# Kernel tuning notes

Hardware: AMD Instinct MI355X
Metric: run time of the kernel (lower is better)

Reference implementation:

```python
import jax, jax.numpy as jnp
import numpy as np

N_NODES = 100000
N_GRAPHS = 1000
NPG = 100           # nodes per graph (fixed)
N_EDGES = 3200000   # avg degree 32
F_IN = 128
K = 30              # SortAggregation k
N_CLASSES = 10


def setup_inputs() -> dict:
    key = jax.random.key(0)
    ks = jax.random.split(key, 24)
    x = jax.random.normal(ks[0], (N_NODES, F_IN), jnp.float32)
    # edges constrained within each 100-node graph
    g = jax.random.randint(ks[1], (N_EDGES,), 0, N_GRAPHS)
    src = g * NPG + jax.random.randint(ks[2], (N_EDGES,), 0, NPG)
    dst = g * NPG + jax.random.randint(ks[3], (N_EDGES,), 0, NPG)
    edge_index = jnp.stack([src, dst]).astype(jnp.int32)
    batch = jnp.repeat(jnp.arange(N_GRAPHS, dtype=jnp.int32), NPG)

    def lin(k, fi, fo):
        return jax.random.normal(k, (fi, fo), jnp.float32) / np.sqrt(fi)

    return {
        "x": x, "edge_index": edge_index, "batch": batch,
        "W1": lin(ks[4], F_IN, 32), "b1": jnp.zeros((32,), jnp.float32),
        "W2": lin(ks[5], 32, 32),   "b2": jnp.zeros((32,), jnp.float32),
        "W3": lin(ks[6], 32, 32),   "b3": jnp.zeros((32,), jnp.float32),
        "W4": lin(ks[7], 32, 1),    "b4": jnp.zeros((1,), jnp.float32),
        "conv5_w": jax.random.normal(ks[8], (16, 1, 97), jnp.float32) / np.sqrt(97.0),
        "conv5_b": jnp.zeros((16,), jnp.float32),
        "conv6_w": jax.random.normal(ks[9], (32, 16, 5), jnp.float32) / np.sqrt(16 * 5.0),
        "conv6_b": jnp.zeros((32,), jnp.float32),
        "fc1_w": lin(ks[10], 352, 128), "fc1_b": jnp.zeros((128,), jnp.float32),
        "fc2_w": lin(ks[11], 128, N_CLASSES), "fc2_b": jnp.zeros((N_CLASSES,), jnp.float32),
    }


def reference(x, edge_index, batch,
              W1, b1, W2, b2, W3, b3, W4, b4,
              conv5_w, conv5_b, conv6_w, conv6_b,
              fc1_w, fc1_b, fc2_w, fc2_b):
    N = x.shape[0]
    src, dst = edge_index[0], edge_index[1]
    # remove_self_loops -> zero edge weight; GCNConv then re-adds self loops (weight 1)
    w = jnp.where(src == dst, 0.0, 1.0).astype(x.dtype)
    deg = jax.ops.segment_sum(w, dst, num_segments=N) + 1.0  # includes self loop
    dis = jax.lax.rsqrt(deg)
    norm = w * dis[src] * dis[dst]        # per-edge D^-1/2 A D^-1/2
    self_norm = dis * dis                 # self-loop coefficient 1/deg

    def gcn(h, W, b):
        h = h @ W                                   # [N, out]
        agg = jax.ops.segment_sum(norm[:, None] * h[src], dst, num_segments=N)
        return agg + self_norm[:, None] * h + b

    x1 = jnp.tanh(gcn(x, W1, b1))
    x2 = jnp.tanh(gcn(x1, W2, b2))
    x3 = jnp.tanh(gcn(x2, W3, b3))
    x4 = jnp.tanh(gcn(x3, W4, b4))
    h = jnp.concatenate([x1, x2, x3, x4], axis=-1)  # [N, 97]
    C = h.shape[-1]

    # SortAggregation(k=30): per graph, sort nodes by last channel descending, keep top k
    xs = h.reshape(N_GRAPHS, NPG, C)
    order = jnp.argsort(-xs[..., -1], axis=1)[:, :K]            # [B, K]
    pooled = jnp.take_along_axis(xs, order[:, :, None], axis=1)  # [B, K, C]
    y = pooled.reshape(N_GRAPHS, 1, K * C)                       # [B, 1, 2910]

    dn = ('NCH', 'OIH', 'NCH')
    y = jax.lax.conv_general_dilated(y, conv5_w, (97,), 'VALID', dimension_numbers=dn)
    y = jax.nn.relu(y + conv5_b[None, :, None])                  # [B, 16, 30]
    B, Co, L = y.shape
    y = y.reshape(B, Co, L // 2, 2).max(axis=-1)                 # maxpool(2,2) -> [B,16,15]
    y = jax.lax.conv_general_dilated(y, conv6_w, (1,), 'VALID', dimension_numbers=dn)
    y = jax.nn.relu(y + conv6_b[None, :, None])                  # [B, 32, 11]
    y = y.reshape(B, -1)                                         # [B, 352]
    out = jax.nn.relu(y @ fc1_w + fc1_b)                         # dropout = identity (eval)
    return jax.nn.log_softmax(out @ fc2_w + fc2_b, axis=-1)
```

## Files before the change

### kernel.cpp

```cpp
#include <hip/hip_runtime.h>

#define N_GRAPHS_C 1000
#define NPG_C      100
#define N_EDGES_C  3200000
#define KTOP_C     30
#define CAP        4096
#define NB_BUCKET  391

typedef _Float16 f16x8 __attribute__((ext_vector_type(8)));
typedef float    f32x4 __attribute__((ext_vector_type(4)));

__device__ __forceinline__ unsigned packh2(float x, float y) {
    _Float16 hx = (_Float16)x, hy = (_Float16)y;
    return (unsigned)__builtin_bit_cast(unsigned short, hx) |
           ((unsigned)__builtin_bit_cast(unsigned short, hy) << 16);
}

__device__ __forceinline__ float f16b(unsigned v) {
    return (float)__builtin_bit_cast(_Float16, (unsigned short)v);
}

__device__ __forceinline__ float ftanh(float x) {
    float e = __expf(2.0f * x);
    return 1.0f - 2.0f * __builtin_amdgcn_rcpf(e + 1.0f);
}

__device__ __forceinline__ void split8(const float* v, f16x8& h, f16x8& l) {
    #pragma unroll
    for (int j = 0; j < 8; ++j) {
        _Float16 hh = (_Float16)v[j];
        h[j] = hh;
        l[j] = (_Float16)(v[j] - (float)hh);
    }
}


__global__ __launch_bounds__(1024)
void bucket_kernel(const int* __restrict__ src, const int* __restrict__ dst,
                   int* __restrict__ gcur, unsigned short* __restrict__ slots,
                   const float* __restrict__ W1, const float* __restrict__ W2,
                   const float* __restrict__ W3, unsigned* __restrict__ wp) {
    const int tid = threadIdx.x;
    if (blockIdx.x == NB_BUCKET) {
        for (int w = tid; w < 2048; w += 1024) {
            int n = w >> 6, kp = w & 63, k = kp * 2;
            float a = W1[k*32 + n], b = W1[(k+1)*32 + n];
            _Float16 ah = (_Float16)a, bh = (_Float16)b;
            wp[w]        = (unsigned)__builtin_bit_cast(unsigned short, ah) |
                           ((unsigned)__builtin_bit_cast(unsigned short, bh) << 16);
            wp[2048 + w] = packh2(a - (float)ah, b - (float)bh);
        }
        for (int w = tid; w < 512; w += 1024) {
            int n = w >> 4, kp = w & 15, k = kp * 2;
            float a = W2[k*32 + n], b = W2[(k+1)*32 + n];
            _Float16 ah = (_Float16)a, bh = (_Float16)b;
            wp[4096 + w] = (unsigned)__builtin_bit_cast(unsigned short, ah) |
                           ((unsigned)__builtin_bit_cast(unsigned short, bh) << 16);
            wp[4608 + w] = packh2(a - (float)ah, b - (float)bh);
            float a3 = W3[k*32 + n], b3v = W3[(k+1)*32 + n];
            _Float16 a3h = (_Float16)a3, b3h = (_Float16)b3v;
            wp[5120 + w] = (unsigned)__builtin_bit_cast(unsigned short, a3h) |
                           ((unsigned)__builtin_bit_cast(unsigned short, b3h) << 16);
            wp[5632 + w] = packh2(a3 - (float)a3h, b3v - (float)b3h);
        }
        return;
    }

    __shared__ int hist[N_GRAPHS_C];
    const int base = blockIdx.x * 8192;
    for (int i = tid; i < N_GRAPHS_C; i += 1024) hist[i] = 0;
    __syncthreads();

    int g[8]; unsigned short pk[8]; bool v[8];
    #pragma unroll
    for (int k = 0; k < 8; ++k) {
        int e = base + tid + k * 1024;
        v[k] = false;
        if (e < N_EDGES_C) {
            int s = src[e], d = dst[e];
            if (s != d) {
                int gg = s / NPG_C;
                g[k] = gg;
                pk[k] = (unsigned short)(((d - gg * NPG_C) << 7) | (s - gg * NPG_C));
                v[k] = true;
                atomicAdd(&hist[gg], 1);
            }
        }
    }
    __syncthreads();
    for (int i = tid; i < N_GRAPHS_C; i += 1024) {
        int c = hist[i];
        hist[i] = atomicAdd(&gcur[i], c);
    }
    __syncthreads();
    #pragma unroll
    for (int k = 0; k < 8; ++k) {
        if (v[k]) {
            int pos = atomicAdd(&hist[g[k]], 1);
            if (pos < CAP) slots[g[k] * CAP + pos] = pk[k];
        }
    }
}

#define SMEM_WORDS 8496

extern "C" __global__ __launch_bounds__(512, 8)
void dgcnn_kernel(const float* __restrict__ x,
                  const int* __restrict__ gcur, const unsigned short* __restrict__ slots,
                  const unsigned* __restrict__ wp,
                  const float* __restrict__ b1, const float* __restrict__ b2,
                  const float* __restrict__ b3,
                  const float* __restrict__ W4, const float* __restrict__ b4,
                  const float* __restrict__ w5, const float* __restrict__ b5,
                  const float* __restrict__ w6, const float* __restrict__ b6,
                  const float* __restrict__ fw1, const float* __restrict__ fb1,
                  const float* __restrict__ fw2, const float* __restrict__ fb2,
                  float* __restrict__ out)
{
    extern __shared__ unsigned smu[];
    unsigned* planes = smu;
    float* xrows  = (float*)(smu + 4352);
    float* pooled = (float*)(smu + 4352);
    float* dis = (float*)(smu + 7952);
    float* t4  = (float*)(smu + 8064);
    unsigned* t4h = smu + 8168;
    unsigned* t4l = smu + 8232;
    float* sX4 = (float*)(smu + 8296);
    int*   srank = (int*)(smu + 8396);
    float* s5  = (float*)smu;
    float* sPb = s5 + 480;
    float* s6  = s5 + 720;
    float* sO1 = s5 + 1072;
    float* sFc = s5 + 1200;
    float* sZ  = s5 + 1712;

    const int tid = threadIdx.x;
    const int g   = blockIdx.x;
    const int l64 = tid & 63;
    const int wv  = tid >> 6;

    const float* xg = x + (size_t)g * NPG_C * 128;
    const unsigned* w1h = wp;
    const unsigned* w1l = wp + 2048;

    for (int idx = tid; idx < 2600; idx += 512) planes[idx] = 0u;
    if (tid < 12) dis[100 + tid] = 0.f;
    if (tid < 100) srank[tid] = 0;
    __syncthreads();

    {
        int ec = gcur[g]; if (ec > CAP) ec = CAP;
        for (int k = tid; k < ec; k += 512) {
            unsigned e = slots[g * CAP + k];
            unsigned idx = (e >> 7) * 104 + (e & 127);
            atomicAdd(&planes[idx >> 2], 1u << ((idx & 3) * 8));
        }
    }
    __syncthreads();

    if (tid < 400) {
        int row = tid >> 2, part = tid & 3;
        int wb = part * 7, we = (part == 3) ? 26 : wb + 7;
        const unsigned* rw = planes + row * 26;
        unsigned s = 0;
        for (int k = wb; k < we; ++k) {
            unsigned v = rw[k];
            s += (v & 0xffu) + ((v >> 8) & 0xffu) + ((v >> 16) & 0xffu) + (v >> 24);
        }
        atomicAdd(&srank[row], (int)s);
    }
    f16x8 afr[4];
    {
        const int arow = (wv << 4) + (l64 & 15);
        if (wv < 7 && arow < 100) {
            const unsigned* cb = planes + arow * 26 + ((l64 >> 4) << 1);
            #pragma unroll
            for (int ks = 0; ks < 4; ++ks) {
                uint2 cw = *(const uint2*)(cb + ks * 8);
                #pragma unroll
                for (int j = 0; j < 4; ++j) {
                    afr[ks][j]     = (_Float16)(float)((cw.x >> (8*j)) & 255u);
                    afr[ks][4 + j] = (_Float16)(float)((cw.y >> (8*j)) & 255u);
                }
            }
        } else {
            #pragma unroll
            for (int ks = 0; ks < 4; ++ks)
                #pragma unroll
                for (int j = 0; j < 8; ++j) afr[ks][j] = (_Float16)0.f;
        }
    }
    __syncthreads();

    if (tid < 100) dis[tid] = rsqrtf((float)srank[tid] + 1.0f);
    __syncthreads();

    auto packStore = [&](f32x4 c, int n, int r0, float4 dv) {
        float v0 = c[0]*dv.x, v1 = c[1]*dv.y, v2 = c[2]*dv.z, v3 = c[3]*dv.w;
        _Float16 h0=(_Float16)v0, h1=(_Float16)v1, h2=(_Float16)v2, h3=(_Float16)v3;
        uint2 wh, wl;
        wh.x = (unsigned)__builtin_bit_cast(unsigned short,h0) |
               ((unsigned)__builtin_bit_cast(unsigned short,h1) << 16);
        wh.y = (unsigned)__builtin_bit_cast(unsigned short,h2) |
               ((unsigned)__builtin_bit_cast(unsigned short,h3) << 16);
        wl.x = packh2(v0-(float)h0, v1-(float)h1);
        wl.y = packh2(v2-(float)h2, v3-(float)h3);
        *(uint2*)&planes[n*68 + (r0>>1)] = wh;
        *(uint2*)&planes[2176 + n*68 + (r0>>1)] = wl;
    };

    for (int idx = tid; idx < 768; idx += 512) {
        int rw = idx / 12, wd = idx - rw * 12;
        planes[rw * 68 + 56 + wd] = 0u;
    }
    if (wv < 7) {
        f32x4 c0 = {0.f,0.f,0.f,0.f}, c1 = {0.f,0.f,0.f,0.f};
        const int arow = (wv << 4) + (l64 & 15);
        const int kq   = (l64 >> 4) << 3;
        const int bn   = l64 & 15;
        const bool aok = arow < 100;
        #pragma unroll
        for (int kc = 0; kc < 4; ++kc) {
            const int kb = (kc << 5) + kq;
            f16x8 ah, al;
            if (aok) {
                float av[8];
                float4 xa = *(const float4*)&xg[arow*128 + kb];
                float4 xb = *(const float4*)&xg[arow*128 + kb + 4];
                av[0]=xa.x; av[1]=xa.y; av[2]=xa.z; av[3]=xa.w;
                av[4]=xb.x; av[5]=xb.y; av[6]=xb.z; av[7]=xb.w;
                split8(av, ah, al);
            } else {
                #pragma unroll
                for (int j = 0; j < 8; ++j) { ah[j] = (_Float16)0.f; al[j] = (_Float16)0.f; }
            }
            f16x8 b0h = __builtin_bit_cast(f16x8, *(const uint4*)(w1h + bn*64 + (kb>>1)));
            f16x8 b0l = __builtin_bit_cast(f16x8, *(const uint4*)(w1l + bn*64 + (kb>>1)));
            f16x8 b1h = __builtin_bit_cast(f16x8, *(const uint4*)(w1h + (bn+16)*64 + (kb>>1)));
            f16x8 b1l = __builtin_bit_cast(f16x8, *(const uint4*)(w1l + (bn+16)*64 + (kb>>1)));
            c0 = __builtin_amdgcn_mfma_f32_16x16x32_f16(ah, b0h, c0, 0, 0, 0);
            c0 = __builtin_amdgcn_mfma_f32_16x16x32_f16(al, b0h, c0, 0, 0, 0);
            c0 = __builtin_amdgcn_mfma_f32_16x16x32_f16(ah, b0l, c0, 0, 0, 0);
            c1 = __builtin_amdgcn_mfma_f32_16x16x32_f16(ah, b1h, c1, 0, 0, 0);
            c1 = __builtin_amdgcn_mfma_f32_16x16x32_f16(al, b1h, c1, 0, 0, 0);
            c1 = __builtin_amdgcn_mfma_f32_16x16x32_f16(ah, b1l, c1, 0, 0, 0);
        }
        const int r0 = (wv << 4) + ((l64 >> 4) << 2);
        float4 dv = *(const float4*)&dis[r0];
        packStore(c0, bn,      r0, dv);
        packStore(c1, bn + 16, r0, dv);
    }
    __syncthreads();

    auto AGG = [&](f32x4& fa, f32x4& fb, const float* Bp, bool wx) {
        if (wv < 7) {
            f32x4 a0 = {0.f,0.f,0.f,0.f}, a1 = {0.f,0.f,0.f,0.f};
            const unsigned* bb = planes + (l64 & 15) * 68 + ((l64 >> 4) << 2);
            #pragma unroll
            for (int p = 0; p < 2; ++p) {
                const unsigned* bp = bb + p * 2176;
                #pragma unroll
                for (int ks = 0; ks < 4; ++ks) {
                    f16x8 b0 = __builtin_bit_cast(f16x8, *(const uint4*)(bp + ks*16));
                    f16x8 b1 = __builtin_bit_cast(f16x8, *(const uint4*)(bp + 16*68 + ks*16));
                    a0 = __builtin_amdgcn_mfma_f32_16x16x32_f16(afr[ks], b0, a0, 0, 0, 0);
                    a1 = __builtin_amdgcn_mfma_f32_16x16x32_f16(afr[ks], b1, a1, 0, 0, 0);
                }
            }
            int n0 = l64 & 15, r0 = (wv << 4) + ((l64 >> 4) << 2);
            uint2 sh0 = *(const uint2*)(planes + n0 * 68 + (r0 >> 1));
            uint2 sl0 = *(const uint2*)(planes + 2176 + n0 * 68 + (r0 >> 1));
            uint2 sh1 = *(const uint2*)(planes + (16 + n0) * 68 + (r0 >> 1));
            uint2 sl1 = *(const uint2*)(planes + 2176 + (16 + n0) * 68 + (r0 >> 1));
            float4 dv = *(const float4*)&dis[r0];
            float bi0 = Bp[n0], bi1 = Bp[16 + n0];
            #pragma unroll
            for (int j = 0; j < 4; ++j) {
                unsigned sft = (unsigned)((j & 1) * 16);
                float sc0 = f16b(((j < 2) ? sh0.x : sh0.y) >> sft) +
                            f16b(((j < 2) ? sl0.x : sl0.y) >> sft);
                float sc1 = f16b(((j < 2) ? sh1.x : sh1.y) >> sft) +
                            f16b(((j < 2) ? sl1.x : sl1.y) >> sft);
                float d_ = (j == 0) ? dv.x : (j == 1) ? dv.y : (j == 2) ? dv.z : dv.w;
                float v0 = ftanh(d_ * (a0[j] + sc0) + bi0);
                float v1 = ftanh(d_ * (a1[j] + sc1) + bi1);
                fa[j] = v0; fb[j] = v1;
                if (wx) {
                    int row = r0 + j;
                    if (row < 100) { xrows[row*36 + n0] = v0; xrows[row*36 + 16 + n0] = v1; }
                }
            }
        }
    };

    auto XWm = [&](const unsigned* wh, const unsigned* wl) {
        if (wv < 7) {
            f32x4 c0 = {0.f,0.f,0.f,0.f}, c1 = {0.f,0.f,0.f,0.f};
            const int arow = (wv << 4) + (l64 & 15);
            const int kq   = (l64 >> 4) << 3;
            const int bn   = l64 & 15;
            f16x8 ah, al;
            if (arow < 100) {
                float av[8];
                float4 xa = *(const float4*)&xrows[arow*36 + kq];
                float4 xb = *(const float4*)&xrows[arow*36 + kq + 4];
                av[0]=xa.x; av[1]=xa.y; av[2]=xa.z; av[3]=xa.w;
                av[4]=xb.x; av[5]=xb.y; av[6]=xb.z; av[7]=xb.w;
                split8(av, ah, al);
            } else {
                #pragma unroll
                for (int j = 0; j < 8; ++j) { ah[j] = (_Float16)0.f; al[j] = (_Float16)0.f; }
            }
            f16x8 b0h = __builtin_bit_cast(f16x8, *(const uint4*)(wh + bn*16 + (kq>>1)));
            f16x8 b0l = __builtin_bit_cast(f16x8, *(const uint4*)(wl + bn*16 + (kq>>1)));
            f16x8 b1h = __builtin_bit_cast(f16x8, *(const uint4*)(wh + (bn+16)*16 + (kq>>1)));
            f16x8 b1l = __builtin_bit_cast(f16x8, *(const uint4*)(wl + (bn+16)*16 + (kq>>1)));
            c0 = __builtin_amdgcn_mfma_f32_16x16x32_f16(ah, b0h, c0, 0, 0, 0);
            c0 = __builtin_amdgcn_mfma_f32_16x16x32_f16(al, b0h, c0, 0, 0, 0);
            c0 = __builtin_amdgcn_mfma_f32_16x16x32_f16(ah, b0l, c0, 0, 0, 0);
            c1 = __builtin_amdgcn_mfma_f32_16x16x32_f16(ah, b1h, c1, 0, 0, 0);
            c1 = __builtin_amdgcn_mfma_f32_16x16x32_f16(al, b1h, c1, 0, 0, 0);
            c1 = __builtin_amdgcn_mfma_f32_16x16x32_f16(ah, b1l, c1, 0, 0, 0);
            const int r0 = (wv << 4) + ((l64 >> 4) << 2);
            float4 dv = *(const float4*)&dis[r0];
            packStore(c0, bn,      r0, dv);
            packStore(c1, bn + 16, r0, dv);
        }
    };

    f32x4 f1a, f1b, f2a, f2b, f3a, f3b;

    AGG(f1a, f1b, b1, true);        __syncthreads();
    XWm(wp + 4096, wp + 4608);      __syncthreads();
    AGG(f2a, f2b, b2, true);        __syncthreads();
    XWm(wp + 5120, wp + 5632);      __syncthreads();
    AGG(f3a, f3b, b3, false);

    if (wv < 7) {
        float w4a = W4[l64 & 15], w4b = W4[16 + (l64 & 15)];
        int r0 = (wv << 4) + ((l64 >> 4) << 2);
        #pragma unroll
        for (int j = 0; j < 4; ++j) {
            float v = f3a[j] * w4a + f3b[j] * w4b;
            v += __shfl_xor(v, 1, 16); v += __shfl_xor(v, 2, 16);
            v += __shfl_xor(v, 4, 16); v += __shfl_xor(v, 8, 16);
            int row = r0 + j;
            if ((l64 & 15) == 0 && row < 100) t4[row] = v * dis[row];
        }
    }
    __syncthreads();

    if (tid < 64) {
        float a = (2*tid < 100) ? t4[2*tid] : 0.f;
        float b = (2*tid+1 < 100) ? t4[2*tid+1] : 0.f;
        _Float16 ah = (_Float16)a, bh = (_Float16)b;
        t4h[tid] = (unsigned)__builtin_bit_cast(unsigned short, ah) |
                   ((unsigned)__builtin_bit_cast(unsigned short, bh) << 16);
        t4l[tid] = packh2(a - (float)ah, b - (float)bh);
    }
    if (tid < 100) srank[tid] = 0;
    __syncthreads();

    if (wv < 7) {
        f32x4 c = {0.f,0.f,0.f,0.f};
        const int kq2 = (l64 >> 4) << 2;
        const bool bz = (l64 & 15) == 0;
        #pragma unroll
        for (int ks = 0; ks < 4; ++ks) {
            f16x8 bh, bl;
            if (bz) {
                bh = __builtin_bit_cast(f16x8, *(const uint4*)(t4h + ks*16 + kq2));
                bl = __builtin_bit_cast(f16x8, *(const uint4*)(t4l + ks*16 + kq2));
            } else {
                #pragma unroll
                for (int j = 0; j < 8; ++j) { bh[j] = (_Float16)0.f; bl[j] = (_Float16)0.f; }
            }
            c = __builtin_amdgcn_mfma_f32_16x16x32_f16(afr[ks], bh, c, 0, 0, 0);
            c = __builtin_amdgcn_mfma_f32_16x16x32_f16(afr[ks], bl, c, 0, 0, 0);
        }
        if (bz) {
            int r0 = (wv << 4) + ((l64 >> 4) << 2);
            #pragma unroll
            for (int j = 0; j < 4; ++j) {
                int row = r0 + j;
                if (row < 100) sX4[row] = tanhf(dis[row] * (c[j] + t4[row]) + b4[0]);
            }
        }
    }
    __syncthreads();

    if (tid < 500) {
        int i = tid / 5, seg = tid - i * 5;
        float vi = sX4[i];
        int c = 0, jb = seg * 20;
        #pragma unroll
        for (int jo = 0; jo < 20; ++jo) {
            int j = jb + jo;
            float vj = sX4[j];
            c += (vj > vi) || (vj == vi && j < i);
        }
        atomicAdd(&srank[i], c);
    }
    __syncthreads();

    if (wv < 7) {
        int n0 = l64 & 15, r0 = (wv << 4) + ((l64 >> 4) << 2);
        #pragma unroll
        for (int j = 0; j < 4; ++j) {
            int row = r0 + j;
            if (row < 100) {
                int rk = srank[row];
                if (rk < KTOP_C) {
                    float* pr = pooled + rk * 100;
                    pr[n0]      = f1a[j]; pr[16 + n0] = f1b[j];
                    pr[32 + n0] = f2a[j]; pr[48 + n0] = f2b[j];
                    pr[64 + n0] = f3a[j]; pr[80 + n0] = f3b[j];
                    if (n0 == 0) pr[96] = sX4[row];
                }
            }
        }
    }
    __syncthreads();

    if (tid < 480) {
        int l = tid >> 4, co = tid & 15;
        const float* pr = pooled + l * 100;
        const float* wr = w5 + co * 97;
        float acc = b5[co];
        for (int c4 = 0; c4 < 96; c4 += 4) {
            const float4 pv = *(const float4*)&pr[c4];
            acc = fmaf(pv.x, wr[c4+0], fmaf(pv.y, wr[c4+1], fmaf(pv.z, wr[c4+2], fmaf(pv.w, wr[c4+3], acc))));
        }
        acc = fmaf(pr[96], wr[96], acc);
        s5[co * 30 + l] = fmaxf(acc, 0.f);
    }
    __syncthreads();

    if (tid < 240) {
        int co = tid / 15, j = tid - co * 15;
        sPb[co * 15 + j] = fmaxf(s5[co * 30 + 2*j], s5[co * 30 + 2*j + 1]);
    }
    __syncthreads();

    if (tid < 352) {
        int co = tid / 11, l = tid - co * 11;
        float acc = b6[co];
        for (int ci = 0; ci < 16; ++ci) {
            const float* wr = w6 + (co * 16 + ci) * 5;
            const float* pr = sPb + ci * 15 + l;
            acc = fmaf(wr[0], pr[0], fmaf(wr[1], pr[1], fmaf(wr[2], pr[2],
                  fmaf(wr[3], pr[3], fmaf(wr[4], pr[4], acc)))));
        }
        s6[co * 11 + l] = fmaxf(acc, 0.f);
    }
    __syncthreads();

    {
        int j = tid & 127, part = tid >> 7;
        int ibeg = part * 88, iend = ibeg + 88;
        float acc = (part == 0) ? fb1[j] : 0.f;
        for (int i = ibeg; i < iend; ++i)
            acc = fmaf(s6[i], fw1[i * 128 + j], acc);
        sFc[part * 128 + j] = acc;
    }
    __syncthreads();
    if (tid < 128) {
        float v = sFc[tid] + sFc[128 + tid] + sFc[256 + tid] + sFc[384 + tid];
        sO1[tid] = fmaxf(v, 0.f);
    }
    __syncthreads();

    if (tid < 10) {
        float acc = fb2[tid];
        for (int k = 0; k < 128; ++k)
            acc = fmaf(sO1[k], fw2[k * 10 + tid], acc);
        sZ[tid] = acc;
    }
    __syncthreads();
    if (tid < 10) {
        float m = sZ[0];
        for (int c = 1; c < 10; ++c) m = fmaxf(m, sZ[c]);
        float se = 0.f;
        for (int c = 0; c < 10; ++c) se += expf(sZ[c] - m);
        out[g * 10 + tid] = sZ[tid] - m - logf(se);
    }
}

extern "C" void kernel_launch(void* const* d_in, const int* in_sizes, int n_in,
                              void* d_out, int out_size, void* d_ws, size_t ws_size,
                              hipStream_t stream) {
    const float* x   = (const float*)d_in[0];
    const int*   ei  = (const int*)d_in[1];
    const int*   src = ei;
    const int*   dst = ei + N_EDGES_C;
    const float* W1 = (const float*)d_in[3];  const float* b1 = (const float*)d_in[4];
    const float* W2 = (const float*)d_in[5];  const float* b2 = (const float*)d_in[6];
    const float* W3 = (const float*)d_in[7];  const float* b3 = (const float*)d_in[8];
    const float* W4 = (const float*)d_in[9];  const float* b4 = (const float*)d_in[10];
    const float* w5 = (const float*)d_in[11]; const float* b5 = (const float*)d_in[12];
    const float* w6 = (const float*)d_in[13]; const float* b6 = (const float*)d_in[14];
    const float* fw1 = (const float*)d_in[15]; const float* fb1 = (const float*)d_in[16];
    const float* fw2 = (const float*)d_in[17]; const float* fb2 = (const float*)d_in[18];
    float* out = (float*)d_out;

    int* gcur = (int*)d_ws;
    unsigned short* slots = (unsigned short*)((char*)d_ws + 4096);
    unsigned* wpp = (unsigned*)((char*)d_ws + 4096 + (size_t)N_GRAPHS_C * CAP * 2);

    hipMemsetAsync(gcur, 0, 4096, stream);

    bucket_kernel<<<NB_BUCKET + 1, 1024, 0, stream>>>(src, dst, gcur, slots,
                                                      W1, W2, W3, wpp);

    size_t smem = (size_t)SMEM_WORDS * sizeof(unsigned);
    hipFuncSetAttribute((const void*)dgcnn_kernel,
                        hipFuncAttributeMaxDynamicSharedMemorySize, (int)smem);
    dgcnn_kernel<<<N_GRAPHS_C, 512, smem, stream>>>(
        x, gcur, slots, wpp, b1, b2, b3, W4, b4,
        w5, b5, w6, b6, fw1, fb1, fw2, fb2, out);
}
```

Measured before the change: 106.0 us.

## Double-buffer GCN feature planes to drop barriers and fuse conv5 with maxpool

New measurement: 104.9 us. Within noise of the previous version (-1.1%).

```diff
diff --git a/kernel.cpp b/kernel.cpp
--- a/kernel.cpp
+++ b/kernel.cpp
@@ -102,9 +102,9 @@
     }
 }
 
-#define SMEM_WORDS 8496
-
-extern "C" __global__ __launch_bounds__(512, 8)
+#define SMEM_WORDS 12848
+
+extern "C" __global__ __launch_bounds__(512, 6)
 void dgcnn_kernel(const float* __restrict__ x,
                   const int* __restrict__ gcur, const unsigned short* __restrict__ slots,
                   const unsigned* __restrict__ wp,
@@ -118,21 +118,21 @@
                   float* __restrict__ out)
 {
     extern __shared__ unsigned smu[];
-    unsigned* planes = smu;
-    float* xrows  = (float*)(smu + 4352);
-    float* pooled = (float*)(smu + 4352);
-    float* dis = (float*)(smu + 7952);
-    float* t4  = (float*)(smu + 8064);
-    unsigned* t4h = smu + 8168;
-    unsigned* t4l = smu + 8232;
-    float* sX4 = (float*)(smu + 8296);
-    int*   srank = (int*)(smu + 8396);
-    float* s5  = (float*)smu;
-    float* sPb = s5 + 480;
-    float* s6  = s5 + 720;
-    float* sO1 = s5 + 1072;
-    float* sFc = s5 + 1200;
-    float* sZ  = s5 + 1712;
+    unsigned* bufA = smu;
+    unsigned* bufB = smu + 4352;
+    float* xrows  = (float*)(smu + 8704);
+    float* pooled = (float*)(smu + 8704);
+    float* dis = (float*)(smu + 12304);
+    float* t4  = (float*)(smu + 12416);
+    unsigned* t4h = smu + 12520;
+    unsigned* t4l = smu + 12584;
+    float* sX4 = (float*)(smu + 12648);
+    int*   srank = (int*)(smu + 12748);
+    float* sPb = (float*)smu;
+    float* s6  = (float*)smu + 240;
+    float* sO1 = (float*)smu + 592;
+    float* sFc = (float*)smu + 720;
+    float* sZ  = (float*)smu + 1232;
 
     const int tid = threadIdx.x;
     const int g   = blockIdx.x;
@@ -143,7 +143,7 @@
     const unsigned* w1h = wp;
     const unsigned* w1l = wp + 2048;
 
-    for (int idx = tid; idx < 2600; idx += 512) planes[idx] = 0u;
+    for (int idx = tid; idx < 2600; idx += 512) bufA[idx] = 0u;
     if (tid < 12) dis[100 + tid] = 0.f;
     if (tid < 100) srank[tid] = 0;
     __syncthreads();
@@ -153,7 +153,7 @@
         for (int k = tid; k < ec; k += 512) {
             unsigned e = slots[g * CAP + k];
             unsigned idx = (e >> 7) * 104 + (e & 127);
-            atomicAdd(&planes[idx >> 2], 1u << ((idx & 3) * 8));
+            atomicAdd(&bufA[idx >> 2], 1u << ((idx & 3) * 8));
         }
     }
     __syncthreads();
@@ -161,7 +161,7 @@
     if (tid < 400) {
         int row = tid >> 2, part = tid & 3;
         int wb = part * 7, we = (part == 3) ? 26 : wb + 7;
-        const unsigned* rw = planes + row * 26;
+        const unsigned* rw = bufA + row * 26;
         unsigned s = 0;
         for (int k = wb; k < we; ++k) {
             unsigned v = rw[k];
@@ -173,7 +173,7 @@
     {
         const int arow = (wv << 4) + (l64 & 15);
         if (wv < 7 && arow < 100) {
-            const unsigned* cb = planes + arow * 26 + ((l64 >> 4) << 1);
+            const unsigned* cb = bufA + arow * 26 + ((l64 >> 4) << 1);
             #pragma unroll
             for (int ks = 0; ks < 4; ++ks) {
                 uint2 cw = *(const uint2*)(cb + ks * 8);
@@ -195,7 +195,7 @@
     if (tid < 100) dis[tid] = rsqrtf((float)srank[tid] + 1.0f);
     __syncthreads();
 
-    auto packStore = [&](f32x4 c, int n, int r0, float4 dv) {
+    auto packStore = [&](unsigned* buf, f32x4 c, int n, int r0, float4 dv) {
         float v0 = c[0]*dv.x, v1 = c[1]*dv.y, v2 = c[2]*dv.z, v3 = c[3]*dv.w;
         _Float16 h0=(_Float16)v0, h1=(_Float16)v1, h2=(_Float16)v2, h3=(_Float16)v3;
         uint2 wh, wl;
@@ -205,13 +205,15 @@
                ((unsigned)__builtin_bit_cast(unsigned short,h3) << 16);
         wl.x = packh2(v0-(float)h0, v1-(float)h1);
         wl.y = packh2(v2-(float)h2, v3-(float)h3);
-        *(uint2*)&planes[n*68 + (r0>>1)] = wh;
-        *(uint2*)&planes[2176 + n*68 + (r0>>1)] = wl;
+        *(uint2*)&buf[n*68 + (r0>>1)] = wh;
+        *(uint2*)&buf[2176 + n*68 + (r0>>1)] = wl;
     };
 
-    for (int idx = tid; idx < 768; idx += 512) {
-        int rw = idx / 12, wd = idx - rw * 12;
-        planes[rw * 68 + 56 + wd] = 0u;
+    for (int idx = tid; idx < 1536; idx += 512) {
+        int b = idx >> 9;
+        int r = idx & 511;
+        int rw = (b * 512 + r) / 12, wd = (b * 512 + r) % 12;
+        if (rw < 64) bufA[rw * 68 + 56 + wd] = 0u; else bufB[(rw - 64) * 68 + 56 + wd] = 0u;
     }
     if (wv < 7) {
         f32x4 c0 = {0.f,0.f,0.f,0.f}, c1 = {0.f,0.f,0.f,0.f};
@@ -247,15 +249,15 @@
         }
         const int r0 = (wv << 4) + ((l64 >> 4) << 2);
         float4 dv = *(const float4*)&dis[r0];
-        packStore(c0, bn,      r0, dv);
-        packStore(c1, bn + 16, r0, dv);
-    }
-    __syncthreads();
-
-    auto AGG = [&](f32x4& fa, f32x4& fb, const float* Bp, bool wx) {
+        packStore(bufA, c0, bn,      r0, dv);
+        packStore(bufA, c1, bn + 16, r0, dv);
+    }
+    __syncthreads();
+
+    auto AGG = [&](const unsigned* buf, f32x4& fa, f32x4& fb, const float* Bp, bool wx) {
         if (wv < 7) {
             f32x4 a0 = {0.f,0.f,0.f,0.f}, a1 = {0.f,0.f,0.f,0.f};
-            const unsigned* bb = planes + (l64 & 15) * 68 + ((l64 >> 4) << 2);
+            const unsigned* bb = buf + (l64 & 15) * 68 + ((l64 >> 4) << 2);
             #pragma unroll
             for (int p = 0; p < 2; ++p) {
                 const unsigned* bp = bb + p * 2176;
@@ -268,10 +270,10 @@
                 }
             }
             int n0 = l64 & 15, r0 = (wv << 4) + ((l64 >> 4) << 2);
-            uint2 sh0 = *(const uint2*)(planes + n0 * 68 + (r0 >> 1));
-            uint2 sl0 = *(const uint2*)(planes + 2176 + n0 * 68 + (r0 >> 1));
-            uint2 sh1 = *(const uint2*)(planes + (16 + n0) * 68 + (r0 >> 1));
-            uint2 sl1 = *(const uint2*)(planes + 2176 + (16 + n0) * 68 + (r0 >> 1));
+            uint2 sh0 = *(const uint2*)(buf + n0 * 68 + (r0 >> 1));
+            uint2 sl0 = *(const uint2*)(buf + 2176 + n0 * 68 + (r0 >> 1));
+            uint2 sh1 = *(const uint2*)(buf + (16 + n0) * 68 + (r0 >> 1));
+            uint2 sl1 = *(const uint2*)(buf + 2176 + (16 + n0) * 68 + (r0 >> 1));
             float4 dv = *(const float4*)&dis[r0];
             float bi0 = Bp[n0], bi1 = Bp[16 + n0];
             #pragma unroll
@@ -293,7 +295,7 @@
         }
     };
 
-    auto XWm = [&](const unsigned* wh, const unsigned* wl) {
+    auto XWm = [&](unsigned* bufDst, const unsigned* wh, const unsigned* wl) {
         if (wv < 7) {
             f32x4 c0 = {0.f,0.f,0.f,0.f}, c1 = {0.f,0.f,0.f,0.f};
             const int arow = (wv << 4) + (l64 & 15);
@@ -323,18 +325,20 @@
             c1 = __builtin_amdgcn_mfma_f32_16x16x32_f16(ah, b1l, c1, 0, 0, 0);
             const int r0 = (wv << 4) + ((l64 >> 4) << 2);
             float4 dv = *(const float4*)&dis[r0];
-            packStore(c0, bn,      r0, dv);
-            packStore(c1, bn + 16, r0, dv);
+            packStore(bufDst, c0, bn,      r0, dv);
+            packStore(bufDst, c1, bn + 16, r0, dv);
         }
     };
 
     f32x4 f1a, f1b, f2a, f2b, f3a, f3b;
 
-    AGG(f1a, f1b, b1, true);        __syncthreads();
-    XWm(wp + 4096, wp + 4608);      __syncthreads();
-    AGG(f2a, f2b, b2, true);        __syncthreads();
-    XWm(wp + 5120, wp + 5632);      __syncthreads();
-    AGG(f3a, f3b, b3, false);
+    AGG(bufA, f1a, f1b, b1, true);
+    XWm(bufB, wp + 4096, wp + 4608);
+    __syncthreads();
+    AGG(bufB, f2a, f2b, b2, true);
+    XWm(bufA, wp + 5120, wp + 5632);
+    __syncthreads();
+    AGG(bufA, f3a, f3b, b3, false);
 
     if (wv < 7) {
         float w4a = W4[l64 & 15], w4b = W4[16 + (l64 & 15)];
@@ -422,23 +426,21 @@
     }
     __syncthreads();
 
-    if (tid < 480) {
-        int l = tid >> 4, co = tid & 15;
-        const float* pr = pooled + l * 100;
+    if (tid < 240) {
+        int l2 = tid >> 4, co = tid & 15;
         const float* wr = w5 + co * 97;
-        float acc = b5[co];
-        for (int c4 = 0; c4 < 96; c4 += 4) {
-            const float4 pv = *(const float4*)&pr[c4];
-            acc = fmaf(pv.x, wr[c4+0], fmaf(pv.y, wr[c4+1], fmaf(pv.z, wr[c4+2], fmaf(pv.w, wr[c4+3], acc))));
-        }
-        acc = fmaf(pr[96], wr[96], acc);
-        s5[co * 30 + l] = fmaxf(acc, 0.f);
-    }
-    __syncthreads();
-
-    if (tid < 240) {
-        int co = tid / 15, j = tid - co * 15;
-        sPb[co * 15 + j] = fmaxf(s5[co * 30 + 2*j], s5[co * 30 + 2*j + 1]);
+        float accs[2];
+        #pragma unroll
+        for (int t = 0; t < 2; ++t) {
+            const float* pr = pooled + (2*l2 + t) * 100;
+            float acc = b5[co];
+            for (int c4 = 0; c4 < 96; c4 += 4) {
+                const float4 pv = *(const float4*)&pr[c4];
+                acc = fmaf(pv.x, wr[c4+0], fmaf(pv.y, wr[c4+1], fmaf(pv.z, wr[c4+2], fmaf(pv.w, wr[c4+3], acc))));
+            }
+            accs[t] = fmaf(pr[96], wr[96], acc);
+        }
+        sPb[co * 15 + l2] = fmaxf(fmaxf(accs[0], accs[1]), 0.f);
     }
     __syncthreads();
 
```

## Separate edge-count buffer, merge barriers into XWm, fuse conv5 with maxpool

Applied to the files above, without the earlier changes.

New measurement: 106.1 us. No clear change (+0.1%).

```diff
diff --git a/kernel.cpp b/kernel.cpp
--- a/kernel.cpp
+++ b/kernel.cpp
@@ -119,6 +119,7 @@
 {
     extern __shared__ unsigned smu[];
     unsigned* planes = smu;
+    unsigned* cnt    = smu + 4352;
     float* xrows  = (float*)(smu + 4352);
     float* pooled = (float*)(smu + 4352);
     float* dis = (float*)(smu + 7952);
@@ -127,12 +128,11 @@
     unsigned* t4l = smu + 8232;
     float* sX4 = (float*)(smu + 8296);
     int*   srank = (int*)(smu + 8396);
-    float* s5  = (float*)smu;
-    float* sPb = s5 + 480;
-    float* s6  = s5 + 720;
-    float* sO1 = s5 + 1072;
-    float* sFc = s5 + 1200;
-    float* sZ  = s5 + 1712;
+    float* sPb = (float*)smu;
+    float* s6  = (float*)smu + 240;
+    float* sO1 = (float*)smu + 592;
+    float* sFc = (float*)smu + 720;
+    float* sZ  = (float*)smu + 1232;
 
     const int tid = threadIdx.x;
     const int g   = blockIdx.x;
@@ -143,7 +143,7 @@
     const unsigned* w1h = wp;
     const unsigned* w1l = wp + 2048;
 
-    for (int idx = tid; idx < 2600; idx += 512) planes[idx] = 0u;
+    for (int idx = tid; idx < 2600; idx += 512) cnt[idx] = 0u;
     if (tid < 12) dis[100 + tid] = 0.f;
     if (tid < 100) srank[tid] = 0;
     __syncthreads();
@@ -153,7 +153,7 @@
         for (int k = tid; k < ec; k += 512) {
             unsigned e = slots[g * CAP + k];
             unsigned idx = (e >> 7) * 104 + (e & 127);
-            atomicAdd(&planes[idx >> 2], 1u << ((idx & 3) * 8));
+            atomicAdd(&cnt[idx >> 2], 1u << ((idx & 3) * 8));
         }
     }
     __syncthreads();
@@ -161,7 +161,7 @@
     if (tid < 400) {
         int row = tid >> 2, part = tid & 3;
         int wb = part * 7, we = (part == 3) ? 26 : wb + 7;
-        const unsigned* rw = planes + row * 26;
+        const unsigned* rw = cnt + row * 26;
         unsigned s = 0;
         for (int k = wb; k < we; ++k) {
             unsigned v = rw[k];
@@ -169,30 +169,13 @@
         }
         atomicAdd(&srank[row], (int)s);
     }
-    f16x8 afr[4];
-    {
-        const int arow = (wv << 4) + (l64 & 15);
-        if (wv < 7 && arow < 100) {
-            const unsigned* cb = planes + arow * 26 + ((l64 >> 4) << 1);
-            #pragma unroll
-            for (int ks = 0; ks < 4; ++ks) {
-                uint2 cw = *(const uint2*)(cb + ks * 8);
-                #pragma unroll
-                for (int j = 0; j < 4; ++j) {
-                    afr[ks][j]     = (_Float16)(float)((cw.x >> (8*j)) & 255u);
-                    afr[ks][4 + j] = (_Float16)(float)((cw.y >> (8*j)) & 255u);
-                }
-            }
-        } else {
-            #pragma unroll
-            for (int ks = 0; ks < 4; ++ks)
-                #pragma unroll
-                for (int j = 0; j < 8; ++j) afr[ks][j] = (_Float16)0.f;
-        }
-    }
     __syncthreads();
 
     if (tid < 100) dis[tid] = rsqrtf((float)srank[tid] + 1.0f);
+    for (int idx = tid; idx < 768; idx += 512) {
+        int rw = idx / 12, wd = idx - rw * 12;
+        planes[rw * 68 + 56 + wd] = 0u;
+    }
     __syncthreads();
 
     auto packStore = [&](f32x4 c, int n, int r0, float4 dv) {
@@ -209,85 +192,105 @@
         *(uint2*)&planes[2176 + n*68 + (r0>>1)] = wl;
     };
 
-    for (int idx = tid; idx < 768; idx += 512) {
-        int rw = idx / 12, wd = idx - rw * 12;
-        planes[rw * 68 + 56 + wd] = 0u;
-    }
     if (wv < 7) {
-        f32x4 c0 = {0.f,0.f,0.f,0.f}, c1 = {0.f,0.f,0.f,0.f};
         const int arow = (wv << 4) + (l64 & 15);
         const int kq   = (l64 >> 4) << 3;
         const int bn   = l64 & 15;
         const bool aok = arow < 100;
-        #pragma unroll
-        for (int kc = 0; kc < 4; ++kc) {
-            const int kb = (kc << 5) + kq;
-            f16x8 ah, al;
-            if (aok) {
-                float av[8];
-                float4 xa = *(const float4*)&xg[arow*128 + kb];
-                float4 xb = *(const float4*)&xg[arow*128 + kb + 4];
-                av[0]=xa.x; av[1]=xa.y; av[2]=xa.z; av[3]=xa.w;
-                av[4]=xb.x; av[5]=xb.y; av[6]=xb.z; av[7]=xb.w;
-                split8(av, ah, al);
-            } else {
-                #pragma unroll
-                for (int j = 0; j < 8; ++j) { ah[j] = (_Float16)0.f; al[j] = (_Float16)0.f; }
-            }
-            f16x8 b0h = __builtin_bit_cast(f16x8, *(const uint4*)(w1h + bn*64 + (kb>>1)));
-            f16x8 b0l = __builtin_bit_cast(f16x8, *(const uint4*)(w1l + bn*64 + (kb>>1)));
-            f16x8 b1h = __builtin_bit_cast(f16x8, *(const uint4*)(w1h + (bn+16)*64 + (kb>>1)));
-            f16x8 b1l = __builtin_bit_cast(f16x8, *(const uint4*)(w1l + (bn+16)*64 + (kb>>1)));
-            c0 = __builtin_amdgcn_mfma_f32_16x16x32_f16(ah, b0h, c0, 0, 0, 0);
-            c0 = __builtin_amdgcn_mfma_f32_16x16x32_f16(al, b0h, c0, 0, 0, 0);
-            c0 = __builtin_amdgcn_mfma_f32_16x16x32_f16(ah, b0l, c0, 0, 0, 0);
-            c1 = __builtin_amdgcn_mfma_f32_16x16x32_f16(ah, b1h, c1, 0, 0, 0);
-            c1 = __builtin_amdgcn_mfma_f32_16x16x32_f16(al, b1h, c1, 0, 0, 0);
-            c1 = __builtin_amdgcn_mfma_f32_16x16x32_f16(ah, b1l, c1, 0, 0, 0);
-        }
         const int r0 = (wv << 4) + ((l64 >> 4) << 2);
         float4 dv = *(const float4*)&dis[r0];
-        packStore(c0, bn,      r0, dv);
-        packStore(c1, bn + 16, r0, dv);
+        #pragma unroll
+        for (int t = 0; t < 2; ++t) {
+            f32x4 c = {0.f,0.f,0.f,0.f};
+            const unsigned* wph = w1h + (bn + 16*t) * 64;
+            const unsigned* wpl = w1l + (bn + 16*t) * 64;
+            #pragma unroll
+            for (int kc = 0; kc < 4; ++kc) {
+                const int kb = (kc << 5) + kq;
+                f16x8 ah, al;
+                if (aok) {
+                    float av[8];
+                    float4 xa = *(const float4*)&xg[arow*128 + kb];
+                    float4 xb = *(const float4*)&xg[arow*128 + kb + 4];
+                    av[0]=xa.x; av[1]=xa.y; av[2]=xa.z; av[3]=xa.w;
+                    av[4]=xb.x; av[5]=xb.y; av[6]=xb.z; av[7]=xb.w;
+                    split8(av, ah, al);
+                } else {
+                    #pragma unroll
+                    for (int j = 0; j < 8; ++j) { ah[j] = (_Float16)0.f; al[j] = (_Float16)0.f; }
+                }
+                f16x8 bh = __builtin_bit_cast(f16x8, *(const uint4*)(wph + (kb>>1)));
+                f16x8 bl = __builtin_bit_cast(f16x8, *(const uint4*)(wpl + (kb>>1)));
+                c = __builtin_amdgcn_mfma_f32_16x16x32_f16(ah, bh, c, 0, 0, 0);
+                c = __builtin_amdgcn_mfma_f32_16x16x32_f16(al, bh, c, 0, 0, 0);
+                c = __builtin_amdgcn_mfma_f32_16x16x32_f16(ah, bl, c, 0, 0, 0);
+            }
+            packStore(c, bn + 16*t, r0, dv);
+        }
+    }
+    f16x8 afr[4];
+    {
+        const int arow = (wv << 4) + (l64 & 15);
+        if (wv < 7 && arow < 100) {
+            const unsigned* cb = cnt + arow * 26 + ((l64 >> 4) << 1);
+            #pragma unroll
+            for (int ks = 0; ks < 4; ++ks) {
+                uint2 cw = *(const uint2*)(cb + ks * 8);
+                #pragma unroll
+                for (int j = 0; j < 4; ++j) {
+                    afr[ks][j]     = (_Float16)(float)((cw.x >> (8*j)) & 255u);
+                    afr[ks][4 + j] = (_Float16)(float)((cw.y >> (8*j)) & 255u);
+                }
+            }
+        } else {
+            #pragma unroll
+            for (int ks = 0; ks < 4; ++ks)
+                #pragma unroll
+                for (int j = 0; j < 8; ++j) afr[ks][j] = (_Float16)0.f;
+        }
     }
     __syncthreads();
 
     auto AGG = [&](f32x4& fa, f32x4& fb, const float* Bp, bool wx) {
         if (wv < 7) {
-            f32x4 a0 = {0.f,0.f,0.f,0.f}, a1 = {0.f,0.f,0.f,0.f};
-            const unsigned* bb = planes + (l64 & 15) * 68 + ((l64 >> 4) << 2);
+            const int n0 = l64 & 15, r0 = (wv << 4) + ((l64 >> 4) << 2);
+            const int kw = (l64 >> 4) << 2;
+            float4 dv = *(const float4*)&dis[r0];
             #pragma unroll
-            for (int p = 0; p < 2; ++p) {
-                const unsigned* bp = bb + p * 2176;
+            for (int t = 0; t < 2; ++t) {
+                f32x4 a = {0.f,0.f,0.f,0.f};
+                const unsigned* bb = planes + (16*t + n0) * 0 + (n0)*0;
+                (void)bb;
                 #pragma unroll
-                for (int ks = 0; ks < 4; ++ks) {
-                    f16x8 b0 = __builtin_bit_cast(f16x8, *(const uint4*)(bp + ks*16));
-                    f16x8 b1 = __builtin_bit_cast(f16x8, *(const uint4*)(bp + 16*68 + ks*16));
-                    a0 = __builtin_amdgcn_mfma_f32_16x16x32_f16(afr[ks], b0, a0, 0, 0, 0);
-                    a1 = __builtin_amdgcn_mfma_f32_16x16x32_f16(afr[ks], b1, a1, 0, 0, 0);
+                for (int p = 0; p < 2; ++p) {
+                    const unsigned* bp = planes + p * 2176 + (16*t + (n0 & 15)) * 0;
+                    (void)bp;
+                    const unsigned* bq = planes + p * 2176 + ( (t == 0) ? n0 : (16 + n0) ) * 0;
+                    (void)bq;
+                    const unsigned* br = planes + p * 2176;
+                    #pragma unroll
+                    for (int ks = 0; ks < 4; ++ks) {
+                        f16x8 bfrag = __builtin_bit_cast(f16x8,
+                            *(const uint4*)(br + ( (l64 & 15) + 16*t ) * 0 + (l64 & 15) * 68 + 16*t*68 + kw + ks*16));
+                        a = __builtin_amdgcn_mfma_f32_16x16x32_f16(afr[ks], bfrag, a, 0, 0, 0);
+                    }
                 }
-            }
-            int n0 = l64 & 15, r0 = (wv << 4) + ((l64 >> 4) << 2);
-            uint2 sh0 = *(const uint2*)(planes + n0 * 68 + (r0 >> 1));
-            uint2 sl0 = *(const uint2*)(planes + 2176 + n0 * 68 + (r0 >> 1));
-            uint2 sh1 = *(const uint2*)(planes + (16 + n0) * 68 + (r0 >> 1));
-            uint2 sl1 = *(const uint2*)(planes + 2176 + (16 + n0) * 68 + (r0 >> 1));
-            float4 dv = *(const float4*)&dis[r0];
-            float bi0 = Bp[n0], bi1 = Bp[16 + n0];
-            #pragma unroll
-            for (int j = 0; j < 4; ++j) {
-                unsigned sft = (unsigned)((j & 1) * 16);
-                float sc0 = f16b(((j < 2) ? sh0.x : sh0.y) >> sft) +
-                            f16b(((j < 2) ? sl0.x : sl0.y) >> sft);
-                float sc1 = f16b(((j < 2) ? sh1.x : sh1.y) >> sft) +
-                            f16b(((j < 2) ? sl1.x : sl1.y) >> sft);
-                float d_ = (j == 0) ? dv.x : (j == 1) ? dv.y : (j == 2) ? dv.z : dv.w;
-                float v0 = ftanh(d_ * (a0[j] + sc0) + bi0);
-                float v1 = ftanh(d_ * (a1[j] + sc1) + bi1);
-                fa[j] = v0; fb[j] = v1;
-                if (wx) {
-                    int row = r0 + j;
-                    if (row < 100) { xrows[row*36 + n0] = v0; xrows[row*36 + 16 + n0] = v1; }
+                uint2 sh = *(const uint2*)(planes + (16*t + n0) * 68 + (r0 >> 1));
+                uint2 sl = *(const uint2*)(planes + 2176 + (16*t + n0) * 68 + (r0 >> 1));
+                float bi = Bp[16*t + n0];
+                f32x4& fo = t ? fb : fa;
+                #pragma unroll
+                for (int j = 0; j < 4; ++j) {
+                    unsigned sft = (unsigned)((j & 1) * 16);
+                    float sc = f16b(((j < 2) ? sh.x : sh.y) >> sft) +
+                               f16b(((j < 2) ? sl.x : sl.y) >> sft);
+                    float d_ = (j == 0) ? dv.x : (j == 1) ? dv.y : (j == 2) ? dv.z : dv.w;
+                    float v = ftanh(d_ * (a[j] + sc) + bi);
+                    fo[j] = v;
+                    if (wx) {
+                        int row = r0 + j;
+                        if (row < 100) xrows[row*36 + 16*t + n0] = v;
+                    }
                 }
             }
         }
@@ -295,10 +298,11 @@
 
     auto XWm = [&](const unsigned* wh, const unsigned* wl) {
         if (wv < 7) {
-            f32x4 c0 = {0.f,0.f,0.f,0.f}, c1 = {0.f,0.f,0.f,0.f};
             const int arow = (wv << 4) + (l64 & 15);
             const int kq   = (l64 >> 4) << 3;
             const int bn   = l64 & 15;
+            const int r0 = (wv << 4) + ((l64 >> 4) << 2);
+            float4 dv = *(const float4*)&dis[r0];
             f16x8 ah, al;
             if (arow < 100) {
                 float av[8];
@@ -311,29 +315,30 @@
                 #pragma unroll
                 for (int j = 0; j < 8; ++j) { ah[j] = (_Float16)0.f; al[j] = (_Float16)0.f; }
             }
-            f16x8 b0h = __builtin_bit_cast(f16x8, *(const uint4*)(wh + bn*16 + (kq>>1)));
-            f16x8 b0l = __builtin_bit_cast(f16x8, *(const uint4*)(wl + bn*16 + (kq>>1)));
-            f16x8 b1h = __builtin_bit_cast(f16x8, *(const uint4*)(wh + (bn+16)*16 + (kq>>1)));
-            f16x8 b1l = __builtin_bit_cast(f16x8, *(const uint4*)(wl + (bn+16)*16 + (kq>>1)));
-            c0 = __builtin_amdgcn_mfma_f32_16x16x32_f16(ah, b0h, c0, 0, 0, 0);
-            c0 = __builtin_amdgcn_mfma_f32_16x16x32_f16(al, b0h, c0, 0, 0, 0);
-            c0 = __builtin_amdgcn_mfma_f32_16x16x32_f16(ah, b0l, c0, 0, 0, 0);
-            c1 = __builtin_amdgcn_mfma_f32_16x16x32_f16(ah, b1h, c1, 0, 0, 0);
-            c1 = __builtin_amdgcn_mfma_f32_16x16x32_f16(al, b1h, c1, 0, 0, 0);
-            c1 = __builtin_amdgcn_mfma_f32_16x16x32_f16(ah, b1l, c1, 0, 0, 0);
-            const int r0 = (wv << 4) + ((l64 >> 4) << 2);
-            float4 dv = *(const float4*)&dis[r0];
-            packStore(c0, bn,      r0, dv);
-            packStore(c1, bn + 16, r0, dv);
+            __syncthreads();
+            #pragma unroll
+            for (int t = 0; t < 2; ++t) {
+                f32x4 c = {0.f,0.f,0.f,0.f};
+                f16x8 bh = __builtin_bit_cast(f16x8, *(const uint4*)(wh + (bn+16*t)*16 + (kq>>1)));
+                f16x8 bl = __builtin_bit_cast(f16x8, *(const uint4*)(wl + (bn+16*t)*16 + (kq>>1)));
+                c = __builtin_amdgcn_mfma_f32_16x16x32_f16(ah, bh, c, 0, 0, 0);
+                c = __builtin_amdgcn_mfma_f32_16x16x32_f16(al, bh, c, 0, 0, 0);
+                c = __builtin_amdgcn_mfma_f32_16x16x32_f16(ah, bl, c, 0, 0, 0);
+                packStore(c, bn + 16*t, r0, dv);
+            }
+        } else {
+            __syncthreads();
         }
     };
 
     f32x4 f1a, f1b, f2a, f2b, f3a, f3b;
 
-    AGG(f1a, f1b, b1, true);        __syncthreads();
-    XWm(wp + 4096, wp + 4608);      __syncthreads();
-    AGG(f2a, f2b, b2, true);        __syncthreads();
-    XWm(wp + 5120, wp + 5632);      __syncthreads();
+    AGG(f1a, f1b, b1, true);
+    XWm(wp + 4096, wp + 4608);
+    __syncthreads();
+    AGG(f2a, f2b, b2, true);
+    XWm(wp + 5120, wp + 5632);
+    __syncthreads();
     AGG(f3a, f3b, b3, false);
 
     if (wv < 7) {
@@ -422,23 +427,21 @@
     }
     __syncthreads();
 
-    if (tid < 480) {
-        int l = tid >> 4, co = tid & 15;
-        const float* pr = pooled + l * 100;
+    if (tid < 240) {
+        int l2 = tid >> 4, co = tid & 15;
         const float* wr = w5 + co * 97;
-        float acc = b5[co];
-        for (int c4 = 0; c4 < 96; c4 += 4) {
-            const float4 pv = *(const float4*)&pr[c4];
-            acc = fmaf(pv.x, wr[c4+0], fmaf(pv.y, wr[c4+1], fmaf(pv.z, wr[c4+2], fmaf(pv.w, wr[c4+3], acc))));
-        }
-        acc = fmaf(pr[96], wr[96], acc);
-        s5[co * 30 + l] = fmaxf(acc, 0.f);
-    }
-    __syncthreads();
-
-    if (tid < 240) {
-        int co = tid / 15, j = tid - co * 15;
-        sPb[co * 15 + j] = fmaxf(s5[co * 30 + 2*j], s5[co * 30 + 2*j + 1]);
+        float accs[2];
+        #pragma unroll
+        for (int t = 0; t < 2; ++t) {
+            const float* pr = pooled + (2*l2 + t) * 100;
+            float acc = b5[co];
+            for (int c4 = 0; c4 < 96; c4 += 4) {
+                const float4 pv = *(const float4*)&pr[c4];
+                acc = fmaf(pv.x, wr[c4+0], fmaf(pv.y, wr[c4+1], fmaf(pv.z, wr[c4+2], fmaf(pv.w, wr[c4+3], acc))));
+            }
+            accs[t] = fmaf(pr[96], wr[96], acc);
+        }
+        sPb[co * 15 + l2] = fmaxf(fmaxf(accs[0], accs[1]), 0.f);
     }
     __syncthreads();
 
```
